# Optimization experiments

Hardware: AMD Instinct MI355X
Metric: run time of the kernel (lower is better)

The kernel has to match this reference:

```python
import jax, jax.numpy as jnp
import numpy as np

HIDDEN = 4096


def setup_inputs() -> dict:
    key = jax.random.key(0)
    k1, k2 = jax.random.split(key)
    hidden_states = jax.random.normal(k1, (8, 2048, HIDDEN), dtype=jnp.float32)
    # gate_proj ~ N(0, 0.02^2), shape (2*hidden, hidden)
    gate_proj = 0.02 * jax.random.normal(k2, (2 * HIDDEN, HIDDEN), dtype=jnp.float32)
    return {"hidden_states": hidden_states, "gate_proj": gate_proj, "world_size": 8}


def reference(hidden_states, gate_proj, world_size):
    h = gate_proj.shape[1]
    view = hidden_states.reshape(-1, h)                 # [N, h]
    mm = jnp.einsum("nh,oh->no", view, gate_proj)      # [N, 2h]  (x @ W.T)
    n, o = mm.shape
    # reduce-scatter over dim 0 with world_size ranks: sum the per-rank chunks
    out = mm.reshape(world_size, n // world_size, o).sum(axis=0)  # [N/W, 2h]
    return out
```

## Files before the change

### kernel.cpp

```cpp
#include <hip/hip_runtime.h>
#include <hip/hip_bf16.h>


#define HID   4096
#define SEQ   2048
#define WORLD 8
#define OUTD  8192

typedef __bf16 bf16x8 __attribute__((ext_vector_type(8)));
typedef short  s16x8  __attribute__((ext_vector_type(8)));
typedef float  f32x4  __attribute__((ext_vector_type(4)));

typedef const __attribute__((address_space(1))) void* gas1_ptr;
typedef __attribute__((address_space(3))) void*       las3_ptr;

static __device__ __forceinline__ unsigned short f2bf(float f) {
    union { float f; unsigned u; } v; v.f = f;
    unsigned u = v.u;
    u += 0x7fffu + ((u >> 16) & 1u);
    return (unsigned short)(u >> 16);
}

#define RED_BLOCKS  2048
#define CONV_BLOCKS 4096
__global__ void prep_kernel(const float* __restrict__ hs,
                            const float* __restrict__ w,
                            unsigned short* __restrict__ xb,
                            unsigned short* __restrict__ wb) {
    if (blockIdx.x < RED_BLOCKS) {
        const int total4 = SEQ * HID / 4;
        const float4* h4 = (const float4*)hs;
        ushort4* o4 = (ushort4*)xb;
        for (int i = blockIdx.x * blockDim.x + threadIdx.x; i < total4;
             i += RED_BLOCKS * blockDim.x) {
            float4 s = h4[i];
            #pragma unroll
            for (int ww = 1; ww < WORLD; ++ww) {
                float4 t = h4[i + ww * total4];
                s.x += t.x; s.y += t.y; s.z += t.z; s.w += t.w;
            }
            ushort4 o;
            o.x = f2bf(s.x); o.y = f2bf(s.y); o.z = f2bf(s.z); o.w = f2bf(s.w);
            o4[i] = o;
        }
    } else {
        const int total4 = OUTD * HID / 4;
        const float4* w4 = (const float4*)w;
        ushort4* o4 = (ushort4*)wb;
        for (int i = (blockIdx.x - RED_BLOCKS) * blockDim.x + threadIdx.x;
             i < total4; i += CONV_BLOCKS * blockDim.x) {
            float4 s = w4[i];
            ushort4 o;
            o.x = f2bf(s.x); o.y = f2bf(s.y); o.z = f2bf(s.z); o.w = f2bf(s.w);
            o4[i] = o;
        }
    }
}


#define BM 256
#define BN 256
#define BK 64
#define KSTEPS (HID / BK)

__global__ __launch_bounds__(512, 2)
void gemm_bt_kernel(const unsigned short* __restrict__ A,
                    const unsigned short* __restrict__ B,
                    float* __restrict__ C) {
    __shared__ __align__(16) unsigned short lsA[2][BM * BK];
    __shared__ __align__(16) unsigned short lsB[2][BN * BK];

    const int tid  = threadIdx.x;
    const int lane = tid & 63;
    const int wave = tid >> 6;
    const int wm   = wave >> 2;
    const int wn   = wave & 3;

    const int bid   = blockIdx.x;
    const int xcd   = bid & 7;
    const int local = bid >> 3;
    const int bm = (xcd >> 2) * 4 + (local >> 3);
    const int bn = (xcd & 3) * 8 + (local & 7);

    const int subrow = lane >> 3;
    const int slot   = lane & 7;
    const int scol   = (slot ^ subrow) * 8;
    const unsigned short* aBase =
        A + (size_t)(bm * BM + wave * 8 + subrow) * HID + scol;
    const unsigned short* bBase =
        B + (size_t)(bn * BN + wave * 8 + subrow) * HID + scol;
    const int ldsW = wave * 8 * BK;

#define ST_A(buf, ktv, l) __builtin_amdgcn_global_load_lds(                     \
        (gas1_ptr)(aBase + (size_t)(ktv) * BK + (size_t)(l) * 64 * HID),        \
        (las3_ptr)(&lsA[buf][(l) * 64 * BK + ldsW]), 16, 0, 0)
#define ST_B(buf, ktv, l) __builtin_amdgcn_global_load_lds(                     \
        (gas1_ptr)(bBase + (size_t)(ktv) * BK + (size_t)(l) * 64 * HID),        \
        (las3_ptr)(&lsB[buf][(l) * 64 * BK + ldsW]), 16, 0, 0)
#define STG_A(buf, ktv, h) do { ST_A(buf, ktv, 2*(h)); ST_A(buf, ktv, 2*(h)+1); } while (0)
#define STG_B(buf, ktv, h) do { ST_B(buf, ktv, 2*(h)); ST_B(buf, ktv, 2*(h)+1); } while (0)

    const int fr    = lane & 15;
    const int fq    = lane >> 4;
    const int axor  = fr & 7;
    const int koff0 = ((0 + fq) ^ axor) * 8;
    const int koff1 = ((4 + fq) ^ axor) * 8;
    const int aRowB = (wm * 128 + fr) * BK;
    const int bRowB = (wn * 64 + fr) * BK;

#define RD_A(dst, P, mm, koff) dst = __builtin_bit_cast(bf16x8,                 \
        *(const s16x8*)&lsA[P][aRowB + (mm) * 16 * BK + (koff)])
#define RD_B(dst, P, nn, koff) dst = __builtin_bit_cast(bf16x8,                 \
        *(const s16x8*)&lsB[P][bRowB + (nn) * 16 * BK + (koff)])

#define BARRIER() __builtin_amdgcn_s_barrier()
#define LGKM0()   asm volatile("s_waitcnt lgkmcnt(0)" ::: "memory")
#define VMC8()    asm volatile("s_waitcnt vmcnt(8)" ::: "memory")
#define VMC0()    asm volatile("s_waitcnt vmcnt(0)" ::: "memory")
#define PRIO1()   __builtin_amdgcn_s_setprio(1)
#define PRIO0()   __builtin_amdgcn_s_setprio(0)

#define MFMA16(VAx, mb)                                                          \
    PRIO1();                                                                     \
    _Pragma("unroll")                                                            \
    for (int s = 0; s < 2; ++s)                                                  \
        _Pragma("unroll")                                                        \
        for (int m = 0; m < 2; ++m)                                              \
            _Pragma("unroll")                                                    \
            for (int n = 0; n < 4; ++n)                                          \
                acc[(mb) + m][n] = __builtin_amdgcn_mfma_f32_16x16x32_bf16(      \
                    VAx[m][s], vb[n][s], acc[(mb) + m][n], 0, 0, 0);             \
    PRIO0()

#define TILE_SECTION(P, Tnext, ST)                                               \
    RD_B(vb[0][0], P, 0, koff0); RD_B(vb[0][1], P, 0, koff1);                    \
    RD_B(vb[1][0], P, 1, koff0); RD_B(vb[1][1], P, 1, koff1);                    \
    RD_B(vb[2][0], P, 2, koff0); RD_B(vb[2][1], P, 2, koff1);                    \
    RD_B(vb[3][0], P, 3, koff0); RD_B(vb[3][1], P, 3, koff1);                    \
    RD_A(va[0][0], P, 0, koff0); RD_A(va[0][1], P, 0, koff1);                    \
    RD_A(va[1][0], P, 1, koff0); RD_A(va[1][1], P, 1, koff1);                    \
    RD_A(vc[0][0], P, 2, koff0); RD_A(vc[0][1], P, 2, koff1);                    \
    RD_A(vc[1][0], P, 3, koff0); RD_A(vc[1][1], P, 3, koff1);                    \
    MFMA16(va, 0);                                                               \
    RD_A(va[0][0], P, 4, koff0); RD_A(va[0][1], P, 4, koff1);                    \
    RD_A(va[1][0], P, 5, koff0); RD_A(va[1][1], P, 5, koff1);                    \
    MFMA16(vc, 2);                                                               \
    RD_A(vc[0][0], P, 6, koff0); RD_A(vc[0][1], P, 6, koff1);                    \
    RD_A(vc[1][0], P, 7, koff0); RD_A(vc[1][1], P, 7, koff1);                    \
    MFMA16(va, 4);                                                               \
    LGKM0();                                                                     \
    BARRIER();                                                                   \
    if (ST) { STG_A(P, Tnext, 0); STG_A(P, Tnext, 1);                            \
              STG_B(P, Tnext, 0); STG_B(P, Tnext, 1); }                          \
    MFMA16(vc, 6);                                                               \
    if (ST) { VMC8(); } else { VMC0(); }                                         \
    BARRIER()

    f32x4 acc[8][4] = {};
    bf16x8 va[2][2], vc[2][2], vb[4][2];

    STG_A(0, 0, 0); STG_A(0, 0, 1); STG_B(0, 0, 0); STG_B(0, 0, 1);
    STG_A(1, 1, 0); STG_A(1, 1, 1); STG_B(1, 1, 0); STG_B(1, 1, 1);
    VMC8();
    BARRIER();

    #pragma unroll 1
    for (int t = 0; t < KSTEPS; t += 2) {
        const bool s2 = (t + 2 < KSTEPS);
        const bool s3 = (t + 3 < KSTEPS);
        TILE_SECTION(0, t + 2, s2);
        TILE_SECTION(1, t + 3, s3);
    }

    const long crow0 = (long)bm * BM + wm * 128 + fq * 4;
    const long ccol0 = (long)bn * BN + wn * 64 + fr;
    #pragma unroll
    for (int m = 0; m < 8; ++m)
        #pragma unroll
        for (int n = 0; n < 4; ++n)
            #pragma unroll
            for (int j = 0; j < 4; ++j)
                C[(crow0 + m * 16 + j) * OUTD + ccol0 + n * 16] = acc[m][n][j];
}

extern "C" void kernel_launch(void* const* d_in, const int* in_sizes, int n_in,
                              void* d_out, int out_size, void* d_ws, size_t ws_size,
                              hipStream_t stream) {
    const float* hs = (const float*)d_in[0];
    const float* w  = (const float*)d_in[1];
    float* out = (float*)d_out;

    unsigned short* xb = (unsigned short*)d_ws;
    unsigned short* wb = xb + (size_t)SEQ * HID;

    hipLaunchKernelGGL(prep_kernel, dim3(RED_BLOCKS + CONV_BLOCKS), dim3(256),
                       0, stream, hs, w, xb, wb);
    hipLaunchKernelGGL(gemm_bt_kernel, dim3((SEQ / BM) * (OUTD / BN)), dim3(512),
                       0, stream, xb, wb, out);
}
```

Before: 228.2 us.

## Restructure GEMM K-loop into single-barrier prefetch-one-ahead pipeline

```diff
diff --git a/kernel.cpp b/kernel.cpp
--- a/kernel.cpp
+++ b/kernel.cpp
@@ -97,8 +97,10 @@
 #define ST_B(buf, ktv, l) __builtin_amdgcn_global_load_lds(                     \
         (gas1_ptr)(bBase + (size_t)(ktv) * BK + (size_t)(l) * 64 * HID),        \
         (las3_ptr)(&lsB[buf][(l) * 64 * BK + ldsW]), 16, 0, 0)
-#define STG_A(buf, ktv, h) do { ST_A(buf, ktv, 2*(h)); ST_A(buf, ktv, 2*(h)+1); } while (0)
-#define STG_B(buf, ktv, h) do { ST_B(buf, ktv, 2*(h)); ST_B(buf, ktv, 2*(h)+1); } while (0)
+#define STG_A4(buf, ktv) do { ST_A(buf, ktv, 0); ST_A(buf, ktv, 1);             \
+                              ST_A(buf, ktv, 2); ST_A(buf, ktv, 3); } while (0)
+#define STG_B4(buf, ktv) do { ST_B(buf, ktv, 0); ST_B(buf, ktv, 1);             \
+                              ST_B(buf, ktv, 2); ST_B(buf, ktv, 3); } while (0)
 
     const int fr    = lane & 15;
     const int fq    = lane >> 4;
@@ -113,12 +115,10 @@
 #define RD_B(dst, P, nn, koff) dst = __builtin_bit_cast(bf16x8,                 \
         *(const s16x8*)&lsB[P][bRowB + (nn) * 16 * BK + (koff)])
 
-#define BARRIER() __builtin_amdgcn_s_barrier()
-#define LGKM0()   asm volatile("s_waitcnt lgkmcnt(0)" ::: "memory")
-#define VMC8()    asm volatile("s_waitcnt vmcnt(8)" ::: "memory")
-#define VMC0()    asm volatile("s_waitcnt vmcnt(0)" ::: "memory")
-#define PRIO1()   __builtin_amdgcn_s_setprio(1)
-#define PRIO0()   __builtin_amdgcn_s_setprio(0)
+#define BARRIER_M() asm volatile("s_barrier" ::: "memory")
+#define VMC0()      asm volatile("s_waitcnt vmcnt(0)" ::: "memory")
+#define PRIO1()     __builtin_amdgcn_s_setprio(1)
+#define PRIO0()     __builtin_amdgcn_s_setprio(0)
 
 #define MFMA16(VAx, mb)                                                          \
     PRIO1();                                                                     \
@@ -132,44 +132,37 @@
                     VAx[m][s], vb[n][s], acc[(mb) + m][n], 0, 0, 0);             \
     PRIO0()
 
-#define TILE_SECTION(P, Tnext, ST)                                               \
+#define TILE(P, T, HAS1)                                                         \
+    BARRIER_M();                                                                 \
+    if (HAS1) { STG_A4((P) ^ 1, (T) + 1); STG_B4((P) ^ 1, (T) + 1); }            \
     RD_B(vb[0][0], P, 0, koff0); RD_B(vb[0][1], P, 0, koff1);                    \
     RD_B(vb[1][0], P, 1, koff0); RD_B(vb[1][1], P, 1, koff1);                    \
     RD_B(vb[2][0], P, 2, koff0); RD_B(vb[2][1], P, 2, koff1);                    \
     RD_B(vb[3][0], P, 3, koff0); RD_B(vb[3][1], P, 3, koff1);                    \
     RD_A(va[0][0], P, 0, koff0); RD_A(va[0][1], P, 0, koff1);                    \
     RD_A(va[1][0], P, 1, koff0); RD_A(va[1][1], P, 1, koff1);                    \
+    MFMA16(va, 0);                                                               \
     RD_A(vc[0][0], P, 2, koff0); RD_A(vc[0][1], P, 2, koff1);                    \
     RD_A(vc[1][0], P, 3, koff0); RD_A(vc[1][1], P, 3, koff1);                    \
-    MFMA16(va, 0);                                                               \
+    MFMA16(vc, 2);                                                               \
     RD_A(va[0][0], P, 4, koff0); RD_A(va[0][1], P, 4, koff1);                    \
     RD_A(va[1][0], P, 5, koff0); RD_A(va[1][1], P, 5, koff1);                    \
-    MFMA16(vc, 2);                                                               \
+    MFMA16(va, 4);                                                               \
     RD_A(vc[0][0], P, 6, koff0); RD_A(vc[0][1], P, 6, koff1);                    \
     RD_A(vc[1][0], P, 7, koff0); RD_A(vc[1][1], P, 7, koff1);                    \
-    MFMA16(va, 4);                                                               \
-    LGKM0();                                                                     \
-    BARRIER();                                                                   \
-    if (ST) { STG_A(P, Tnext, 0); STG_A(P, Tnext, 1);                            \
-              STG_B(P, Tnext, 0); STG_B(P, Tnext, 1); }                          \
     MFMA16(vc, 6);                                                               \
-    if (ST) { VMC8(); } else { VMC0(); }                                         \
-    BARRIER()
+    if (HAS1) { VMC0(); }
 
     f32x4 acc[8][4] = {};
     bf16x8 va[2][2], vc[2][2], vb[4][2];
 
-    STG_A(0, 0, 0); STG_A(0, 0, 1); STG_B(0, 0, 0); STG_B(0, 0, 1);
-    STG_A(1, 1, 0); STG_A(1, 1, 1); STG_B(1, 1, 0); STG_B(1, 1, 1);
-    VMC8();
-    BARRIER();
+    STG_A4(0, 0); STG_B4(0, 0);
+    VMC0();
 
     #pragma unroll 1
     for (int t = 0; t < KSTEPS; t += 2) {
-        const bool s2 = (t + 2 < KSTEPS);
-        const bool s3 = (t + 3 < KSTEPS);
-        TILE_SECTION(0, t + 2, s2);
-        TILE_SECTION(1, t + 3, s3);
+        TILE(0, t,     true);
+        TILE(1, t + 1, (t + 2 < KSTEPS));
     }
 
     const long crow0 = (long)bm * BM + wm * 128 + fq * 4;
```

Measured after the change: 225.6 us. About the same (-1.2%).
